# Kernel tuning notes

Measured on AMD Instinct MI355X. Metric: run time of the kernel, lower is better.

Reference implementation:

```python
import jax, jax.numpy as jnp
import numpy as np

EMO = 1024
FEAT = 1024
K = 128  # aggregation_k
H_LIST = (4, 8, 16)
D_LIST = tuple(EMO // h for h in H_LIST)  # (256, 128, 64)
D_SUM = sum(D_LIST)  # 448
H_SUM = sum(H_LIST)  # 28
N = len(H_LIST)      # 3 subspaces
TEMP = float(np.power(D_SUM, 0.5))


def _block_mask(sizes, total):
    m = np.zeros((len(sizes), total), np.float32)
    off = 0
    for i, s in enumerate(sizes):
        m[i, off:off + s] = 1.0
        off += s
    return jnp.asarray(m)

M_Q_BLK = _block_mask(D_LIST, D_SUM)  # [N, d_sum]
M_V_BLK = _block_mask(H_LIST, H_SUM)  # [N, h_sum]


def setup_inputs() -> dict:
    key = jax.random.key(0)
    ks = iter(jax.random.split(key, 32))
    nrm = lambda shape, s=1.0: jax.random.normal(next(ks), shape, jnp.float32) * s
    B, Lt, Lp, Nv = 32, 1024, 512, 256
    return {
        "emo_embedding": nrm((B, Lt, EMO)),
        "phr_feat": nrm((B, Lp, FEAT)),
        "video_feat": nrm((B, Nv, FEAT)),
        "w_v_W": nrm((FEAT, FEAT), FEAT ** -0.5), "w_v_b": nrm((FEAT,), 0.01),
        "agg_a_W": nrm((FEAT, K), FEAT ** -0.5), "agg_a_b": nrm((K,), 0.01),
        "agg_c_W": nrm((FEAT, EMO), FEAT ** -0.5), "agg_c_b": nrm((EMO,), 0.01),
        "ele_W": nrm((2 * EMO, 1), (2 * EMO) ** -0.5), "ele_b": nrm((1,), 0.01),
        "wq_W": nrm((EMO, D_SUM), EMO ** -0.5), "wq_b": nrm((D_SUM,), 0.01),
        "wk_W": nrm((EMO, D_SUM), EMO ** -0.5), "wk_b": nrm((D_SUM,), 0.01),
        "wv_W": nrm((EMO, H_SUM), EMO ** -0.5), "wv_b": nrm((H_SUM,), 0.01),
        "wr_W": nrm((EMO, N), EMO ** -0.5), "wr_b": nrm((N,), 0.01),
    }


def reference(emo_embedding, phr_feat, video_feat,
              w_v_W, w_v_b, agg_a_W, agg_a_b, agg_c_W, agg_c_b,
              ele_W, ele_b, wq_W, wq_b, wk_W, wk_b, wv_W, wv_b, wr_W, wr_b):
    B, Lt, _ = emo_embedding.shape
    Nv = video_feat.shape[1]
    Lp = phr_feat.shape[1]

    # --- feature_aggregation ---
    # AdaptiveAvgPool1d(Nv); Lp % Nv == 0 so it is an exact reshape-mean.
    phr = phr_feat.reshape(B, Nv, Lp // Nv, FEAT).mean(axis=2)
    combine = jnp.concatenate([phr @ w_v_W + w_v_b, video_feat], axis=1)   # [B, 2*Nv, FEAT]
    attn_a = jax.nn.softmax(combine @ agg_a_W + agg_a_b, axis=-1)          # [B, 2*Nv, K]
    agg_feat = jnp.einsum('bmk,bme->bke', attn_a, combine @ agg_c_W + agg_c_b)  # [B, K, EMO]

    # --- element_routing ---
    A_pool = jnp.einsum('ble,bke->blk', emo_embedding, agg_feat).mean(axis=1)   # [B, K]
    route = jnp.einsum('bk,bke->be', A_pool, agg_feat)[:, None, :]              # [B, 1, EMO]
    route = jnp.broadcast_to(route, emo_embedding.shape)
    R_e = jnp.tanh(jnp.concatenate([emo_embedding, route], axis=-1) @ ele_W + ele_b)  # [B, Lt, 1]
    route_emo = R_e * emo_embedding                                              # [B, Lt, EMO]

    # --- subspace_routing ---
    Q = route_emo @ wq_W + wq_b        # [B, Lt, d_sum]
    Kp = agg_feat @ wk_W + wk_b        # [B, K, d_sum]
    V = agg_feat @ wv_W + wv_b         # [B, K, h_sum]
    Rp = agg_feat @ wr_W + wr_b        # [B, K, N]

    # N masked copies of Q (block subspace masks); K/R are plain repeats, V is masked.
    Qm = (Q[:, None] * M_Q_BLK[None, :, None, :]).reshape(B, N * Lt, D_SUM)
    Kf = jnp.tile(Kp, (1, N, 1))                                         # [B, N*K, d_sum]
    Vf = (V[:, None] * M_V_BLK[None, :, None, :]).reshape(B, N * K, H_SUM)
    Rf = jnp.tile(Rp, (1, N, 1))                                         # [B, N*K, N]

    attn = jax.nn.softmax(jnp.einsum('bqd,bkd->bqk', Qm, Kf) / TEMP, axis=-1)  # [B, N*Lt, N*K]
    O = jnp.tanh(attn @ Vf).reshape(B, N, Lt, H_SUM)
    O_R = (attn @ Rf).reshape(B, N, Lt, N)

    # per-subspace head gating of route_emo
    T_list = []
    hoff = 0
    for i in range(N):
        hi, di = H_LIST[i], D_LIST[i]
        ori = route_emo.reshape(B, Lt, hi, di)
        Oi = O[:, i, :, hoff:hoff + hi][..., None]      # [B, Lt, hi, 1]
        T_list.append((ori * Oi).reshape(B, Lt, EMO))
        hoff += hi
    T = jnp.stack(T_list, axis=1)                        # [B, N, Lt, EMO]

    Rdiag = jnp.stack([O_R[:, j, :, j].mean(axis=-1) for j in range(N)], axis=1)  # [B, N]
    gate = jax.nn.softmax(Rdiag, axis=-1)[:, :, None, None]
    return emo_embedding + (gate * T).sum(axis=1)
```

## Files before the change

### kernel.cpp

```cpp
#include <hip/hip_runtime.h>
#include <math.h>

typedef long long i64;
typedef __attribute__((ext_vector_type(8))) short bf16x8;
typedef __attribute__((ext_vector_type(4))) float f32x4;

#define TEMP_ISQ 0.047245559f

__device__ __forceinline__ unsigned short f2b(float x) {
  union { float f; unsigned u; } a; a.f = x;
  return (unsigned short)((a.u + 0x7fffu + ((a.u >> 16) & 1u)) >> 16);
}
__device__ __forceinline__ float b2f(unsigned short b) {
  union { float f; unsigned u; } a; a.u = ((unsigned)b) << 16; return a.f;
}

template<int BIAS, int OUTM, int RS, int BZDIV>
__global__ __launch_bounds__(256)
void gemm_mfma(const unsigned short* __restrict__ Ab, i64 sA,
               const unsigned short* __restrict__ Bb, i64 sB,
               const float* __restrict__ bias,
               void* __restrict__ Ob, i64 sO,
               unsigned short* __restrict__ O2b, i64 sO2,
               int Nn, int Kd, int ldA, int ldB, int ldO,
               const float* __restrict__ rowScale, i64 sRS)
{
  __shared__ unsigned short As[8192];
  __shared__ unsigned short Bs[8192];
  const int tid = threadIdx.x;
  const int w = tid >> 6, lane = tid & 63;

  const int gx = gridDim.x, gy = gridDim.y;
  int nwg = gx * gy * gridDim.z;
  int bid = blockIdx.x + gx * (blockIdx.y + gy * blockIdx.z);
  int L = bid;
  if ((nwg & 7) == 0) L = (bid & 7) * (nwg >> 3) + (bid >> 3);
  const int bx = L % gx;
  int rem = L / gx;
  const int by = rem % gy;
  const int z  = rem / gy;

  const int m0 = by * 128, n0 = bx * 128;
  const unsigned short* A = Ab + (i64)z * sA;
  const unsigned short* B = Bb + (i64)(BZDIV == 1 ? z : z / BZDIV) * sB;
  const int wr = w >> 1, wc = w & 1;
  const int rS = tid >> 3, sS = tid & 7;
  const int cL = lane & 15, sl = lane >> 4;

  f32x4 acc[4][4];
  #pragma unroll
  for (int i = 0; i < 4; ++i)
    #pragma unroll
    for (int j = 0; j < 4; ++j) acc[i][j] = (f32x4){0.f, 0.f, 0.f, 0.f};

  for (int k0 = 0; k0 < Kd; k0 += 64) {
    #pragma unroll
    for (int q = 0; q < 4; ++q) {
      int r = rS + q * 32;
      int sg = sS ^ (r & 7);
      const unsigned short* sa = A + (i64)(m0 + r) * ldA + k0 + sg * 8;
      const unsigned short* sb = B + (i64)(n0 + r) * ldB + k0 + sg * 8;
      __builtin_amdgcn_global_load_lds(
          (__attribute__((address_space(1))) void*)sa,
          (__attribute__((address_space(3))) void*)&As[r * 64 + sS * 8], 16, 0, 0);
      __builtin_amdgcn_global_load_lds(
          (__attribute__((address_space(1))) void*)sb,
          (__attribute__((address_space(3))) void*)&Bs[r * 64 + sS * 8], 16, 0, 0);
    }
    __syncthreads();
    bf16x8 af[2][4], bfv[2][4];
    #pragma unroll
    for (int kk = 0; kk < 2; ++kk) {
      #pragma unroll
      for (int mi = 0; mi < 4; ++mi) {
        int rr = wr * 64 + mi * 16 + cL;
        int ph = (kk * 4 + sl) ^ (rr & 7);
        af[kk][mi] = *(const bf16x8*)&As[rr * 64 + ph * 8];
      }
      #pragma unroll
      for (int ni = 0; ni < 4; ++ni) {
        int rr = wc * 64 + ni * 16 + cL;
        int ph = (kk * 4 + sl) ^ (rr & 7);
        bfv[kk][ni] = *(const bf16x8*)&Bs[rr * 64 + ph * 8];
      }
    }
    #pragma unroll
    for (int kk = 0; kk < 2; ++kk)
      #pragma unroll
      for (int mi = 0; mi < 4; ++mi)
        #pragma unroll
        for (int ni = 0; ni < 4; ++ni)
          acc[mi][ni] = __builtin_amdgcn_mfma_f32_16x16x32_bf16(af[kk][mi], bfv[kk][ni], acc[mi][ni], 0, 0, 0);
    __syncthreads();
  }

  #pragma unroll
  for (int mi = 0; mi < 4; ++mi) {
    const int rowb = m0 + wr * 64 + mi * 16 + sl * 4;
    #pragma unroll
    for (int ni = 0; ni < 4; ++ni) {
      const int col = n0 + wc * 64 + ni * 16 + cL;
      if (col < Nn) {
        float bc = (BIAS == 1) ? bias[col] : 0.f;
        #pragma unroll
        for (int rg = 0; rg < 4; ++rg) {
          float v = acc[mi][ni][rg];
          if (RS) v *= rowScale[(i64)z * sRS + rowb + rg];
          v += bc;
          if (BIAS == 2) v += bias[rowb + rg];
          i64 oidx = (i64)(rowb + rg) * ldO + col;
          if (OUTM == 0)      ((float*)Ob)[(i64)z * sO + oidx] = v;
          else if (OUTM == 1) ((unsigned short*)Ob)[(i64)z * sO + oidx] = f2b(v);
          else if (OUTM == 3) ((float*)Ob)[(i64)z * sO + oidx] = tanhf(v * (1.f / 3.f));
          else {
            ((float*)Ob)[(i64)z * sO + oidx] = v;
            O2b[(i64)z * sO2 + oidx] = f2b(v);
          }
        }
      }
    }
  }
}

__global__ __launch_bounds__(256)
void emo_pass1(const float* __restrict__ emo, const float* __restrict__ eleW,
               unsigned short* __restrict__ emoB, float* __restrict__ colPart,
               float* __restrict__ dotE) {
  int b = blockIdx.y, lc = blockIdx.x;
  int t = threadIdx.x, lane = t & 63, w = t >> 6;
  float4 w4 = ((const float4*)eleW)[t];
  float4 acc = make_float4(0.f, 0.f, 0.f, 0.f);
  __shared__ float dw[64][4];
  const float4* src = (const float4*)emo + ((i64)b * 1024 + lc * 64) * 256;
  ushort4* dst = (ushort4*)emoB + ((i64)b * 1024 + lc * 64) * 256;
  for (int lr = 0; lr < 64; ++lr) {
    float4 v = src[lr * 256 + t];
    acc.x += v.x; acc.y += v.y; acc.z += v.z; acc.w += v.w;
    float d = v.x * w4.x + v.y * w4.y + v.z * w4.z + v.w * w4.w;
    #pragma unroll
    for (int o = 32; o; o >>= 1) d += __shfl_xor(d, o);
    if (!lane) dw[lr][w] = d;
    ushort4 o4; o4.x = f2b(v.x); o4.y = f2b(v.y); o4.z = f2b(v.z); o4.w = f2b(v.w);
    dst[lr * 256 + t] = o4;
  }
  __syncthreads();
  if (t < 64) dotE[(i64)b * 1024 + lc * 64 + t] = dw[t][0] + dw[t][1] + dw[t][2] + dw[t][3];
  ((float4*)colPart)[((i64)b * 16 + lc) * 256 + t] = acc;
}

__global__ void colmean2(const float* __restrict__ colPart, float* __restrict__ emomean) {
  int b = blockIdx.y, e = blockIdx.x * 256 + threadIdx.x;
  float s = 0.f;
  #pragma unroll
  for (int lc = 0; lc < 16; ++lc) s += colPart[((i64)b * 16 + lc) * 1024 + e];
  emomean[b * 1024 + e] = s * (1.f / 1024.f);
}

__global__ __launch_bounds__(256)
void transpose_w(const float* __restrict__ in, unsigned short* __restrict__ out,
                 int Kd, int N, int Npad) {
  __shared__ float T[32][33];
  int n0 = blockIdx.x * 32, k0 = blockIdx.y * 32;
  int t = threadIdx.x;
  #pragma unroll
  for (int p = 0; p < 4; ++p) {
    int idx = t + 256 * p; int kk = idx >> 5, nn = idx & 31;
    float v = 0.f;
    if (n0 + nn < N && k0 + kk < Kd) v = in[(i64)(k0 + kk) * N + (n0 + nn)];
    T[nn][kk] = v;
  }
  __syncthreads();
  #pragma unroll
  for (int p = 0; p < 4; ++p) {
    int idx = t + 256 * p; int nn = idx >> 5, kk = idx & 31;
    if (n0 + nn < Npad && k0 + kk < Kd) out[(i64)(n0 + nn) * Kd + (k0 + kk)] = f2b(T[nn][kk]);
  }
}

__global__ void kvr_bias_kernel(const float* wkb, const float* wvb, const float* wrb, float* out) {
  int t = blockIdx.x * 256 + threadIdx.x;
  if (t >= 480) return;
  out[t] = (t < 448) ? wkb[t] : (t < 476) ? wvb[t - 448] : (t < 479) ? wrb[t - 476] : 0.f;
}

__global__ void pool_phr(const float* __restrict__ phr, unsigned short* __restrict__ out) {
  i64 idx = (i64)blockIdx.x * 256 + threadIdx.x;
  if (idx >= 2097152) return;
  i64 bm = idx >> 8; int c = (int)(idx & 255);
  i64 b = bm >> 8, m = bm & 255;
  const float4* r0 = (const float4*)(phr + (b * 512 + 2 * m) * 1024) + c;
  const float4* r1 = (const float4*)(phr + (b * 512 + 2 * m + 1) * 1024) + c;
  float4 a = *r0, d = *r1;
  ushort4 o;
  o.x = f2b(0.5f * (a.x + d.x)); o.y = f2b(0.5f * (a.y + d.y));
  o.z = f2b(0.5f * (a.z + d.z)); o.w = f2b(0.5f * (a.w + d.w));
  ((ushort4*)out)[idx] = o;
}

__global__ void vconv(const float* __restrict__ video, unsigned short* __restrict__ combine) {
  i64 idx = (i64)blockIdx.x * 256 + threadIdx.x;
  if (idx >= 2097152) return;
  i64 b = idx >> 16, r = idx & 65535;
  float4 v = ((const float4*)video)[idx];
  ushort4 o;
  o.x = f2b(v.x); o.y = f2b(v.y); o.z = f2b(v.z); o.w = f2b(v.w);
  ((ushort4*)combine)[b * 131072 + 65536 + r] = o;
}

__global__ void vt_fill(const unsigned short* __restrict__ KVR, unsigned short* __restrict__ VT) {
  int b = blockIdx.y;
  int idx = blockIdx.x * 256 + threadIdx.x;
  int n = idx >> 7, k = idx & 127;
  unsigned short v = 0;
  if (n < 28) v = KVR[(i64)b * 61440 + k * 480 + 448 + n];
  VT[((i64)b * 128 + n) * 128 + k] = v;
}

__global__ void softmax_attn_a(const float* __restrict__ logits, unsigned short* __restrict__ outT) {
  int gw = (int)(((i64)blockIdx.x * blockDim.x + threadIdx.x) >> 6);
  int lane = threadIdx.x & 63;
  if (gw >= 32 * 512) return;
  int b = gw >> 9, m = gw & 511;
  const float* p = logits + (i64)gw * 128;
  float x0 = p[lane], x1 = p[lane + 64];
  float mx = fmaxf(x0, x1);
  #pragma unroll
  for (int o = 32; o; o >>= 1) mx = fmaxf(mx, __shfl_xor(mx, o));
  float e0 = expf(x0 - mx), e1 = expf(x1 - mx);
  float s = e0 + e1;
  #pragma unroll
  for (int o = 32; o; o >>= 1) s += __shfl_xor(s, o);
  float inv = 1.f / s;
  unsigned short* o0 = outT + (i64)b * 128 * 512 + m;
  o0[(i64)lane * 512] = f2b(e0 * inv);
  o0[(i64)(lane + 64) * 512] = f2b(e1 * inv);
}

__global__ void softmax_P_bf(const unsigned short* __restrict__ PL, unsigned short* __restrict__ P) {
  i64 gw = ((i64)blockIdx.x * blockDim.x + threadIdx.x) >> 6;
  int lane = threadIdx.x & 63;
  if (gw >= 98304) return;
  const unsigned short* p = PL + gw * 128;
  float x0 = b2f(p[lane]) * TEMP_ISQ, x1 = b2f(p[lane + 64]) * TEMP_ISQ;
  float mx = fmaxf(x0, x1);
  #pragma unroll
  for (int o = 32; o; o >>= 1) mx = fmaxf(mx, __shfl_xor(mx, o));
  float e0 = expf(x0 - mx), e1 = expf(x1 - mx);
  float s = e0 + e1;
  #pragma unroll
  for (int o = 32; o; o >>= 1) s += __shfl_xor(s, o);
  float inv = 1.f / s;
  P[gw * 128 + lane] = f2b(e0 * inv);
  P[gw * 128 + lane + 64] = f2b(e1 * inv);
}

__global__ void apool_kernel(const float* __restrict__ emomean, const float* __restrict__ agg,
                             float* __restrict__ Apool) {
  int gw = (int)(((i64)blockIdx.x * blockDim.x + threadIdx.x) >> 6);
  int lane = threadIdx.x & 63;
  if (gw >= 32 * 128) return;
  int b = gw >> 7, k = gw & 127;
  const float* ag = agg + ((i64)b * 128 + k) * 1024;
  const float* em = emomean + (i64)b * 1024;
  float s = 0.f;
  #pragma unroll
  for (int j = 0; j < 16; ++j) { int e = j * 64 + lane; s += em[e] * ag[e]; }
  #pragma unroll
  for (int o = 32; o; o >>= 1) s += __shfl_down(s, o);
  if (!lane) Apool[gw] = s;
}

__global__ void route1_kernel(const float* __restrict__ Apool, const float* __restrict__ agg,
                              float* __restrict__ routePart) {
  int b = blockIdx.z, kc = blockIdx.y;
  int e = blockIdx.x * 256 + threadIdx.x;
  __shared__ float Ap[32];
  if (threadIdx.x < 32) Ap[threadIdx.x] = Apool[b * 128 + kc * 32 + threadIdx.x];
  __syncthreads();
  const float* ag = agg + ((i64)b * 128 + kc * 32) * 1024 + e;
  float s = 0.f;
  #pragma unroll
  for (int k = 0; k < 32; ++k) s += Ap[k] * ag[(i64)k * 1024];
  routePart[((i64)kc * 32 + b) * 1024 + e] = s;
}
__global__ void route2_kernel(const float* __restrict__ routePart, float* __restrict__ route) {
  int b = blockIdx.y, e = blockIdx.x * 256 + threadIdx.x;
  float s = 0.f;
  #pragma unroll
  for (int kc = 0; kc < 4; ++kc) s += routePart[((i64)kc * 32 + b) * 1024 + e];
  route[b * 1024 + e] = s;
}

__global__ void rb_kernel(const float* __restrict__ route, const float* __restrict__ eleW,
                          const float* __restrict__ eleb, float* __restrict__ rb) {
  int b = blockIdx.x, t = threadIdx.x;
  float s = 0.f;
  for (int j = t; j < 1024; j += 256) s += route[b * 1024 + j] * eleW[1024 + j];
  __shared__ float red[256];
  red[t] = s; __syncthreads();
  for (int o = 128; o > 0; o >>= 1) { if (t < o) red[t] += red[t + o]; __syncthreads(); }
  if (t == 0) rb[b] = red[0] + eleb[0];
}

__global__ void re_small(const float* __restrict__ dotE, const float* __restrict__ rb,
                         float* __restrict__ Re) {
  int i = blockIdx.x * 256 + threadIdx.x;
  Re[i] = tanhf(dotE[i] + rb[i >> 10]);
}

__global__ void pmean1_kernel(const unsigned short* __restrict__ P, float* __restrict__ Ppart) {
  int bi = blockIdx.x, c = blockIdx.y, k = threadIdx.x;
  const unsigned short* p = P + ((i64)bi * 1024 + c * 128) * 128 + k;
  float s = 0.f;
  for (int l = 0; l < 128; ++l) s += b2f(p[(i64)l * 128]);
  Ppart[((i64)bi * 8 + c) * 128 + k] = s;
}
__global__ void pmean2_kernel(const float* __restrict__ Ppart, float* __restrict__ Pmean) {
  int bi = blockIdx.x, k = threadIdx.x;
  float s = 0.f;
  #pragma unroll
  for (int c = 0; c < 8; ++c) s += Ppart[((i64)bi * 8 + c) * 128 + k];
  Pmean[bi * 128 + k] = s * (1.f / 1024.f);
}

__global__ void rdiag_gate_kernel(const float* __restrict__ Pmean, const unsigned short* __restrict__ KVR,
                                  float* __restrict__ gate) {
  int b = blockIdx.x, t = threadIdx.x;
  __shared__ float red[128];
  __shared__ float rd[3];
  for (int i = 0; i < 3; ++i) {
    float v = Pmean[((i64)b * 3 + i) * 128 + t] * b2f(KVR[(i64)b * 61440 + t * 480 + 476 + i]);
    red[t] = v; __syncthreads();
    for (int o = 64; o > 0; o >>= 1) { if (t < o) red[t] += red[t + o]; __syncthreads(); }
    if (t == 0) rd[i] = red[0];
    __syncthreads();
  }
  if (t == 0) {
    float m = fmaxf(rd[0], fmaxf(rd[1], rd[2]));
    float e0 = expf(rd[0] - m), e1 = expf(rd[1] - m), e2 = expf(rd[2] - m);
    float inv = 1.f / (e0 + e1 + e2);
    gate[b * 3 + 0] = e0 * inv; gate[b * 3 + 1] = e1 * inv; gate[b * 3 + 2] = e2 * inv;
  }
}

__global__ __launch_bounds__(256)
void final_kernel(const unsigned short* __restrict__ emoB, const float* __restrict__ Re,
                  const float* __restrict__ O, const float* __restrict__ gate,
                  float* __restrict__ out) {
  i64 bl = blockIdx.x;
  int b = (int)(bl >> 10), l = (int)(bl & 1023);
  __shared__ float Gg[16];
  int t = threadIdx.x;
  if (t < 16) {
    float g0 = gate[b * 3], g1 = gate[b * 3 + 1], g2 = gate[b * 3 + 2];
    float o0 = O[((i64)(b * 3 + 0) * 1024 + l) * 28 + (t >> 2)];
    float o1 = O[((i64)(b * 3 + 1) * 1024 + l) * 28 + 4 + (t >> 1)];
    float o2 = O[((i64)(b * 3 + 2) * 1024 + l) * 28 + 12 + t];
    Gg[t] = g0 * o0 + g1 * o1 + g2 * o2;
  }
  __syncthreads();
  float re = Re[bl];
  ushort4 e4 = ((const ushort4*)(emoB + bl * 1024))[t];
  float g = 1.f + re * Gg[t >> 4];
  ((float4*)(out + bl * 1024))[t] =
      make_float4(b2f(e4.x) * g, b2f(e4.y) * g, b2f(e4.z) * g, b2f(e4.w) * g);
}

extern "C" void kernel_launch(void* const* d_in, const int* in_sizes, int n_in,
                              void* d_out, int out_size, void* d_ws, size_t ws_size,
                              hipStream_t stream) {
  const float* emo     = (const float*)d_in[0];
  const float* phr     = (const float*)d_in[1];
  const float* video   = (const float*)d_in[2];
  const float* w_v_W   = (const float*)d_in[3];
  const float* w_v_b   = (const float*)d_in[4];
  const float* agg_a_W = (const float*)d_in[5];
  const float* agg_a_b = (const float*)d_in[6];
  const float* agg_c_W = (const float*)d_in[7];
  const float* agg_c_b = (const float*)d_in[8];
  const float* ele_W   = (const float*)d_in[9];
  const float* ele_b   = (const float*)d_in[10];
  const float* wq_W    = (const float*)d_in[11];
  const float* wq_b    = (const float*)d_in[12];
  const float* wk_W    = (const float*)d_in[13];
  const float* wk_b    = (const float*)d_in[14];
  const float* wv_W    = (const float*)d_in[15];
  const float* wv_b    = (const float*)d_in[16];
  const float* wr_W    = (const float*)d_in[17];
  const float* wr_b    = (const float*)d_in[18];

  char* ws = (char*)d_ws;
  const i64 oEmoB    = 0;
  const i64 oCombine = 67108864;
  const i64 oPL      = 67108864;
  const i64 oPooled  = 100663296;
  const i64 oLogitsA = 100663296;
  const i64 oAggF    = 100663296;
  const i64 oO       = 100663296;
  const i64 oCT      = 117440512;
  const i64 oQ       = 117440512;
  const i64 oAttnAT  = 150994944;
  const i64 oAggB    = 155189248;
  const i64 oWvT     = 163577856;
  const i64 oAaT     = 165675008;
  const i64 oAcT     = 165937152;
  const i64 oWqT     = 168034304;
  const i64 oKvrT    = 169082880;
  const i64 oKVR     = 170131456;
  const i64 oVT      = 174063616;
  const i64 oKvrB    = 175112192;
  const i64 oEmomean = 175116288;
  const i64 oColPart = 175247360;
  const i64 oDotE    = 177344512;
  const i64 oApool   = 177475584;
  const i64 oRoutePt = 177491968;
  const i64 oRoute   = 178016256;
  const i64 oRb      = 178147328;
  const i64 oRe      = 178147584;
  const i64 oPpart   = 178278656;
  const i64 oPmean   = 178671872;
  const i64 oGate    = 178721024;

  unsigned short* emoB    = (unsigned short*)(ws + oEmoB);
  unsigned short* combine = (unsigned short*)(ws + oCombine);
  unsigned short* PL      = (unsigned short*)(ws + oPL);
  unsigned short* P       = PL;
  unsigned short* pooled  = (unsigned short*)(ws + oPooled);
  float*          logitsA = (float*)(ws + oLogitsA);
  float*          aggF    = (float*)(ws + oAggF);
  float*          O       = (float*)(ws + oO);
  unsigned short* CT      = (unsigned short*)(ws + oCT);
  unsigned short* Q       = (unsigned short*)(ws + oQ);
  unsigned short* attnAT  = (unsigned short*)(ws + oAttnAT);
  unsigned short* aggB    = (unsigned short*)(ws + oAggB);
  unsigned short* wvT     = (unsigned short*)(ws + oWvT);
  unsigned short* aaT     = (unsigned short*)(ws + oAaT);
  unsigned short* acT     = (unsigned short*)(ws + oAcT);
  unsigned short* wqT     = (unsigned short*)(ws + oWqT);
  unsigned short* kvrT    = (unsigned short*)(ws + oKvrT);
  unsigned short* KVR     = (unsigned short*)(ws + oKVR);
  unsigned short* VT      = (unsigned short*)(ws + oVT);
  float*          kvrB    = (float*)(ws + oKvrB);
  float*          emomean = (float*)(ws + oEmomean);
  float*          colPart = (float*)(ws + oColPart);
  float*          dotE    = (float*)(ws + oDotE);
  float*          Apool   = (float*)(ws + oApool);
  float*          routePt = (float*)(ws + oRoutePt);
  float*          route   = (float*)(ws + oRoute);
  float*          rbv     = (float*)(ws + oRb);
  float*          Re      = (float*)(ws + oRe);
  float*          Ppart   = (float*)(ws + oPpart);
  float*          Pmean   = (float*)(ws + oPmean);
  float*          gate    = (float*)(ws + oGate);

  dim3 blk(256);

  emo_pass1<<<dim3(16, 32), blk, 0, stream>>>(emo, ele_W, emoB, colPart, dotE);

  transpose_w<<<dim3(32, 32), blk, 0, stream>>>(w_v_W, wvT, 1024, 1024, 1024);
  transpose_w<<<dim3(4, 32),  blk, 0, stream>>>(agg_a_W, aaT, 1024, 128, 128);
  transpose_w<<<dim3(32, 32), blk, 0, stream>>>(agg_c_W, acT, 1024, 1024, 1024);
  transpose_w<<<dim3(16, 32), blk, 0, stream>>>(wq_W, wqT, 1024, 448, 512);
  transpose_w<<<dim3(14, 32), blk, 0, stream>>>(wk_W, kvrT, 1024, 448, 448);
  transpose_w<<<dim3(1, 32),  blk, 0, stream>>>(wv_W, kvrT + (i64)448 * 1024, 1024, 28, 28);
  transpose_w<<<dim3(2, 32),  blk, 0, stream>>>(wr_W, kvrT + (i64)476 * 1024, 1024, 3, 36);
  kvr_bias_kernel<<<2, blk, 0, stream>>>(wk_b, wv_b, wr_b, kvrB);

  pool_phr<<<8192, blk, 0, stream>>>(phr, pooled);
  vconv<<<8192, blk, 0, stream>>>(video, combine);
  gemm_mfma<1, 1, 0, 1><<<dim3(8, 2, 32), blk, 0, stream>>>(pooled, 262144, wvT, 0, w_v_b,
      (void*)combine, 524288, nullptr, 0, 1024, 1024, 1024, 1024, 1024, nullptr, 0);
  gemm_mfma<1, 0, 0, 1><<<dim3(1, 4, 32), blk, 0, stream>>>(combine, 524288, aaT, 0, agg_a_b,
      (void*)logitsA, 65536, nullptr, 0, 128, 1024, 1024, 1024, 128, nullptr, 0);
  softmax_attn_a<<<4096, blk, 0, stream>>>(logitsA, attnAT);
  gemm_mfma<2, 1, 0, 1><<<dim3(4, 8, 32), blk, 0, stream>>>(acT, 0, combine, 524288, agg_c_b,
      (void*)CT, 524288, nullptr, 0, 512, 1024, 1024, 1024, 512, nullptr, 0);
  gemm_mfma<0, 2, 0, 1><<<dim3(8, 1, 32), blk, 0, stream>>>(attnAT, 65536, CT, 524288, nullptr,
      (void*)aggF, 131072, aggB, 131072, 1024, 512, 512, 512, 1024, nullptr, 0);

  colmean2<<<dim3(4, 32), blk, 0, stream>>>(colPart, emomean);
  apool_kernel<<<1024, blk, 0, stream>>>(emomean, aggF, Apool);
  route1_kernel<<<dim3(4, 4, 32), blk, 0, stream>>>(Apool, aggF, routePt);
  route2_kernel<<<dim3(4, 32), blk, 0, stream>>>(routePt, route);
  rb_kernel<<<32, blk, 0, stream>>>(route, ele_W, ele_b, rbv);
  re_small<<<128, blk, 0, stream>>>(dotE, rbv, Re);

  gemm_mfma<1, 1, 0, 1><<<dim3(4, 1, 32), blk, 0, stream>>>(aggB, 131072, kvrT, 0, kvrB,
      (void*)KVR, 61440, nullptr, 0, 480, 1024, 1024, 1024, 480, nullptr, 0);
  vt_fill<<<dim3(64, 32), blk, 0, stream>>>(KVR, VT);
  gemm_mfma<1, 1, 1, 1><<<dim3(4, 8, 32), blk, 0, stream>>>(emoB, 1048576, wqT, 0, wq_b,
      (void*)Q, 458752, nullptr, 0, 448, 1024, 1024, 1024, 448, Re, 1024);

  const int doffs[3] = {0, 256, 384};
  const int kds[3]   = {256, 128, 64};
  for (int i = 0; i < 3; ++i) {
    gemm_mfma<0, 1, 0, 1><<<dim3(1, 8, 32), blk, 0, stream>>>(Q + doffs[i], 458752,
        KVR + doffs[i], 61440, nullptr,
        (void*)(PL + (i64)i * 131072), 393216, nullptr, 0, 128, kds[i], 448, 480, 128, nullptr, 0);
  }
  softmax_P_bf<<<24576, blk, 0, stream>>>(PL, P);
  pmean1_kernel<<<dim3(96, 8), 128, 0, stream>>>(P, Ppart);
  pmean2_kernel<<<96, 128, 0, stream>>>(Ppart, Pmean);
  gemm_mfma<0, 3, 0, 3><<<dim3(1, 8, 96), blk, 0, stream>>>(P, 131072, VT, 16384, nullptr,
      (void*)O, 28672, nullptr, 0, 28, 128, 128, 128, 28, nullptr, 0);
  rdiag_gate_kernel<<<32, 128, 0, stream>>>(Pmean, KVR, gate);
  final_kernel<<<32768, blk, 0, stream>>>(emoB, Re, O, gate, (float*)d_out);
}
```

Baseline: 472.6 us.

## Merge small kernels to cut launch count and widen emo_pass1 grid

```diff
diff --git a/kernel.cpp b/kernel.cpp
--- a/kernel.cpp
+++ b/kernel.cpp
@@ -15,7 +15,7 @@
   union { float f; unsigned u; } a; a.u = ((unsigned)b) << 16; return a.f;
 }
 
-template<int BIAS, int OUTM, int RS, int BZDIV>
+template<int BIAS, int OUTM, int RS, int BZDIV, int XMODE = 0>
 __global__ __launch_bounds__(256)
 void gemm_mfma(const unsigned short* __restrict__ Ab, i64 sA,
                const unsigned short* __restrict__ Bb, i64 sB,
@@ -23,7 +23,8 @@
                void* __restrict__ Ob, i64 sO,
                unsigned short* __restrict__ O2b, i64 sO2,
                int Nn, int Kd, int ldA, int ldB, int ldO,
-               const float* __restrict__ rowScale, i64 sRS)
+               const float* __restrict__ rowScale, i64 sRS,
+               const float* __restrict__ rsAdd)
 {
   __shared__ unsigned short As[8192];
   __shared__ unsigned short Bs[8192];
@@ -41,8 +42,20 @@
   const int z  = rem / gy;
 
   const int m0 = by * 128, n0 = bx * 128;
-  const unsigned short* A = Ab + (i64)z * sA;
-  const unsigned short* B = Bb + (i64)(BZDIV == 1 ? z : z / BZDIV) * sB;
+  const unsigned short* A;
+  const unsigned short* B;
+  int KdL = Kd;
+  if (XMODE == 1) {
+    int bb = z / 3, ii = z - bb * 3;
+    const int dof_[3] = {0, 256, 384};
+    const int kdt_[3] = {256, 128, 64};
+    A = Ab + dof_[ii] + (i64)bb * sA;
+    B = Bb + dof_[ii] + (i64)bb * sB;
+    KdL = kdt_[ii];
+  } else {
+    A = Ab + (i64)z * sA;
+    B = Bb + (i64)(BZDIV == 1 ? z : z / BZDIV) * sB;
+  }
   const int wr = w >> 1, wc = w & 1;
   const int rS = tid >> 3, sS = tid & 7;
   const int cL = lane & 15, sl = lane >> 4;
@@ -53,7 +66,7 @@
     #pragma unroll
     for (int j = 0; j < 4; ++j) acc[i][j] = (f32x4){0.f, 0.f, 0.f, 0.f};
 
-  for (int k0 = 0; k0 < Kd; k0 += 64) {
+  for (int k0 = 0; k0 < KdL; k0 += 64) {
     #pragma unroll
     for (int q = 0; q < 4; ++q) {
       int r = rS + q * 32;
@@ -105,7 +118,7 @@
         #pragma unroll
         for (int rg = 0; rg < 4; ++rg) {
           float v = acc[mi][ni][rg];
-          if (RS) v *= rowScale[(i64)z * sRS + rowb + rg];
+          if (RS) v *= tanhf(rowScale[(i64)z * sRS + rowb + rg] + rsAdd[z]);
           v += bc;
           if (BIAS == 2) v += bias[rowb + rg];
           i64 oidx = (i64)(rowb + rg) * ldO + col;
@@ -130,10 +143,11 @@
   int t = threadIdx.x, lane = t & 63, w = t >> 6;
   float4 w4 = ((const float4*)eleW)[t];
   float4 acc = make_float4(0.f, 0.f, 0.f, 0.f);
-  __shared__ float dw[64][4];
-  const float4* src = (const float4*)emo + ((i64)b * 1024 + lc * 64) * 256;
-  ushort4* dst = (ushort4*)emoB + ((i64)b * 1024 + lc * 64) * 256;
-  for (int lr = 0; lr < 64; ++lr) {
+  __shared__ float dw[16][4];
+  const float4* src = (const float4*)emo + ((i64)b * 1024 + lc * 16) * 256;
+  ushort4* dst = (ushort4*)emoB + ((i64)b * 1024 + lc * 16) * 256;
+  #pragma unroll 4
+  for (int lr = 0; lr < 16; ++lr) {
     float4 v = src[lr * 256 + t];
     acc.x += v.x; acc.y += v.y; acc.z += v.z; acc.w += v.w;
     float d = v.x * w4.x + v.y * w4.y + v.z * w4.z + v.w * w4.w;
@@ -144,36 +158,50 @@
     dst[lr * 256 + t] = o4;
   }
   __syncthreads();
-  if (t < 64) dotE[(i64)b * 1024 + lc * 64 + t] = dw[t][0] + dw[t][1] + dw[t][2] + dw[t][3];
-  ((float4*)colPart)[((i64)b * 16 + lc) * 256 + t] = acc;
+  if (t < 16) dotE[(i64)b * 1024 + lc * 16 + t] = dw[t][0] + dw[t][1] + dw[t][2] + dw[t][3];
+  ((float4*)colPart)[((i64)b * 64 + lc) * 256 + t] = acc;
 }
 
 __global__ void colmean2(const float* __restrict__ colPart, float* __restrict__ emomean) {
   int b = blockIdx.y, e = blockIdx.x * 256 + threadIdx.x;
   float s = 0.f;
-  #pragma unroll
-  for (int lc = 0; lc < 16; ++lc) s += colPart[((i64)b * 16 + lc) * 1024 + e];
+  #pragma unroll 8
+  for (int lc = 0; lc < 64; ++lc) s += colPart[((i64)b * 64 + lc) * 1024 + e];
   emomean[b * 1024 + e] = s * (1.f / 1024.f);
 }
 
 __global__ __launch_bounds__(256)
-void transpose_w(const float* __restrict__ in, unsigned short* __restrict__ out,
-                 int Kd, int N, int Npad) {
+void transpose_all(const float* __restrict__ w_v_W, const float* __restrict__ agg_a_W,
+                   const float* __restrict__ agg_c_W, const float* __restrict__ wq_W,
+                   const float* __restrict__ wk_W, const float* __restrict__ wv_W,
+                   const float* __restrict__ wr_W,
+                   unsigned short* __restrict__ wvT, unsigned short* __restrict__ aaT,
+                   unsigned short* __restrict__ acT, unsigned short* __restrict__ wqT,
+                   unsigned short* __restrict__ kvrT) {
   __shared__ float T[32][33];
-  int n0 = blockIdx.x * 32, k0 = blockIdx.y * 32;
+  int bx = blockIdx.x;
+  const float* in; unsigned short* out; int N, Npad, s0;
+  if (bx < 32)      { in = w_v_W;   out = wvT;                     N = 1024; Npad = 1024; s0 = 0; }
+  else if (bx < 36) { in = agg_a_W; out = aaT;                     N = 128;  Npad = 128;  s0 = 32; }
+  else if (bx < 68) { in = agg_c_W; out = acT;                     N = 1024; Npad = 1024; s0 = 36; }
+  else if (bx < 84) { in = wq_W;    out = wqT;                     N = 448;  Npad = 512;  s0 = 68; }
+  else if (bx < 98) { in = wk_W;    out = kvrT;                    N = 448;  Npad = 448;  s0 = 84; }
+  else if (bx < 99) { in = wv_W;    out = kvrT + (i64)448 * 1024;  N = 28;   Npad = 28;   s0 = 98; }
+  else              { in = wr_W;    out = kvrT + (i64)476 * 1024;  N = 3;    Npad = 36;   s0 = 99; }
+  int n0 = (bx - s0) * 32, k0 = blockIdx.y * 32;
   int t = threadIdx.x;
   #pragma unroll
   for (int p = 0; p < 4; ++p) {
     int idx = t + 256 * p; int kk = idx >> 5, nn = idx & 31;
     float v = 0.f;
-    if (n0 + nn < N && k0 + kk < Kd) v = in[(i64)(k0 + kk) * N + (n0 + nn)];
+    if (n0 + nn < N) v = in[(i64)(k0 + kk) * N + (n0 + nn)];
     T[nn][kk] = v;
   }
   __syncthreads();
   #pragma unroll
   for (int p = 0; p < 4; ++p) {
     int idx = t + 256 * p; int nn = idx >> 5, kk = idx & 31;
-    if (n0 + nn < Npad && k0 + kk < Kd) out[(i64)(n0 + nn) * Kd + (k0 + kk)] = f2b(T[nn][kk]);
+    if (n0 + nn < Npad) out[(i64)(n0 + nn) * 1024 + (k0 + kk)] = f2b(T[nn][kk]);
   }
 }
 
@@ -270,24 +298,17 @@
   if (!lane) Apool[gw] = s;
 }
 
-__global__ void route1_kernel(const float* __restrict__ Apool, const float* __restrict__ agg,
-                              float* __restrict__ routePart) {
-  int b = blockIdx.z, kc = blockIdx.y;
+__global__ void route_kernel(const float* __restrict__ Apool, const float* __restrict__ agg,
+                             float* __restrict__ route) {
+  int b = blockIdx.y;
   int e = blockIdx.x * 256 + threadIdx.x;
-  __shared__ float Ap[32];
-  if (threadIdx.x < 32) Ap[threadIdx.x] = Apool[b * 128 + kc * 32 + threadIdx.x];
+  __shared__ float Ap[128];
+  if (threadIdx.x < 128) Ap[threadIdx.x] = Apool[b * 128 + threadIdx.x];
   __syncthreads();
-  const float* ag = agg + ((i64)b * 128 + kc * 32) * 1024 + e;
+  const float* ag = agg + (i64)b * 128 * 1024 + e;
   float s = 0.f;
-  #pragma unroll
-  for (int k = 0; k < 32; ++k) s += Ap[k] * ag[(i64)k * 1024];
-  routePart[((i64)kc * 32 + b) * 1024 + e] = s;
-}
-__global__ void route2_kernel(const float* __restrict__ routePart, float* __restrict__ route) {
-  int b = blockIdx.y, e = blockIdx.x * 256 + threadIdx.x;
-  float s = 0.f;
-  #pragma unroll
-  for (int kc = 0; kc < 4; ++kc) s += routePart[((i64)kc * 32 + b) * 1024 + e];
+  #pragma unroll 8
+  for (int k = 0; k < 128; ++k) s += Ap[k] * ag[(i64)k * 1024];
   route[b * 1024 + e] = s;
 }
 
@@ -302,12 +323,6 @@
   if (t == 0) rb[b] = red[0] + eleb[0];
 }
 
-__global__ void re_small(const float* __restrict__ dotE, const float* __restrict__ rb,
-                         float* __restrict__ Re) {
-  int i = blockIdx.x * 256 + threadIdx.x;
-  Re[i] = tanhf(dotE[i] + rb[i >> 10]);
-}
-
 __global__ void pmean1_kernel(const unsigned short* __restrict__ P, float* __restrict__ Ppart) {
   int bi = blockIdx.x, c = blockIdx.y, k = threadIdx.x;
   const unsigned short* p = P + ((i64)bi * 1024 + c * 128) * 128 + k;
@@ -315,21 +330,17 @@
   for (int l = 0; l < 128; ++l) s += b2f(p[(i64)l * 128]);
   Ppart[((i64)bi * 8 + c) * 128 + k] = s;
 }
-__global__ void pmean2_kernel(const float* __restrict__ Ppart, float* __restrict__ Pmean) {
-  int bi = blockIdx.x, k = threadIdx.x;
-  float s = 0.f;
-  #pragma unroll
-  for (int c = 0; c < 8; ++c) s += Ppart[((i64)bi * 8 + c) * 128 + k];
-  Pmean[bi * 128 + k] = s * (1.f / 1024.f);
-}
-
-__global__ void rdiag_gate_kernel(const float* __restrict__ Pmean, const unsigned short* __restrict__ KVR,
-                                  float* __restrict__ gate) {
+
+__global__ void pmean2_rdiag(const float* __restrict__ Ppart, const unsigned short* __restrict__ KVR,
+                             float* __restrict__ gate) {
   int b = blockIdx.x, t = threadIdx.x;
   __shared__ float red[128];
   __shared__ float rd[3];
   for (int i = 0; i < 3; ++i) {
-    float v = Pmean[((i64)b * 3 + i) * 128 + t] * b2f(KVR[(i64)b * 61440 + t * 480 + 476 + i]);
+    float s = 0.f;
+    #pragma unroll
+    for (int c = 0; c < 8; ++c) s += Ppart[((i64)(b * 3 + i) * 8 + c) * 128 + t];
+    float v = s * (1.f / 1024.f) * b2f(KVR[(i64)b * 61440 + t * 480 + 476 + i]);
     red[t] = v; __syncthreads();
     for (int o = 64; o > 0; o >>= 1) { if (t < o) red[t] += red[t + o]; __syncthreads(); }
     if (t == 0) rd[i] = red[0];
@@ -344,9 +355,9 @@
 }
 
 __global__ __launch_bounds__(256)
-void final_kernel(const unsigned short* __restrict__ emoB, const float* __restrict__ Re,
-                  const float* __restrict__ O, const float* __restrict__ gate,
-                  float* __restrict__ out) {
+void final_kernel(const unsigned short* __restrict__ emoB, const float* __restrict__ dotE,
+                  const float* __restrict__ rbv, const float* __restrict__ O,
+                  const float* __restrict__ gate, float* __restrict__ out) {
   i64 bl = blockIdx.x;
   int b = (int)(bl >> 10), l = (int)(bl & 1023);
   __shared__ float Gg[16];
@@ -359,7 +370,7 @@
     Gg[t] = g0 * o0 + g1 * o1 + g2 * o2;
   }
   __syncthreads();
-  float re = Re[bl];
+  float re = tanhf(dotE[bl] + rbv[b]);
   ushort4 e4 = ((const ushort4*)(emoB + bl * 1024))[t];
   float g = 1.f + re * Gg[t >> 4];
   ((float4*)(out + bl * 1024))[t] =
@@ -411,15 +422,12 @@
   const i64 oKvrB    = 175112192;
   const i64 oEmomean = 175116288;
   const i64 oColPart = 175247360;
-  const i64 oDotE    = 177344512;
-  const i64 oApool   = 177475584;
-  const i64 oRoutePt = 177491968;
-  const i64 oRoute   = 178016256;
-  const i64 oRb      = 178147328;
-  const i64 oRe      = 178147584;
-  const i64 oPpart   = 178278656;
-  const i64 oPmean   = 178671872;
-  const i64 oGate    = 178721024;
+  const i64 oDotE    = 183635968;
+  const i64 oApool   = 183767040;
+  const i64 oRoute   = 183783424;
+  const i64 oRb      = 183914496;
+  const i64 oPpart   = 183914752;
+  const i64 oGate    = 184307968;
 
   unsigned short* emoB    = (unsigned short*)(ws + oEmoB);
   unsigned short* combine = (unsigned short*)(ws + oCombine);
@@ -445,64 +453,49 @@
   float*          colPart = (float*)(ws + oColPart);
   float*          dotE    = (float*)(ws + oDotE);
   float*          Apool   = (float*)(ws + oApool);
-  float*          routePt = (float*)(ws + oRoutePt);
   float*          route   = (float*)(ws + oRoute);
   float*          rbv     = (float*)(ws + oRb);
-  float*          Re      = (float*)(ws + oRe);
   float*          Ppart   = (float*)(ws + oPpart);
-  float*          Pmean   = (float*)(ws + oPmean);
   float*          gate    = (float*)(ws + oGate);
 
   dim3 blk(256);
 
-  emo_pass1<<<dim3(16, 32), blk, 0, stream>>>(emo, ele_W, emoB, colPart, dotE);
-
-  transpose_w<<<dim3(32, 32), blk, 0, stream>>>(w_v_W, wvT, 1024, 1024, 1024);
-  transpose_w<<<dim3(4, 32),  blk, 0, stream>>>(agg_a_W, aaT, 1024, 128, 128);
-  transpose_w<<<dim3(32, 32), blk, 0, stream>>>(agg_c_W, acT, 1024, 1024, 1024);
-  transpose_w<<<dim3(16, 32), blk, 0, stream>>>(wq_W, wqT, 1024, 448, 512);
-  transpose_w<<<dim3(14, 32), blk, 0, stream>>>(wk_W, kvrT, 1024, 448, 448);
-  transpose_w<<<dim3(1, 32),  blk, 0, stream>>>(wv_W, kvrT + (i64)448 * 1024, 1024, 28, 28);
-  transpose_w<<<dim3(2, 32),  blk, 0, stream>>>(wr_W, kvrT + (i64)476 * 1024, 1024, 3, 36);
+  emo_pass1<<<dim3(64, 32), blk, 0, stream>>>(emo, ele_W, emoB, colPart, dotE);
+
+  transpose_all<<<dim3(101, 32), blk, 0, stream>>>(w_v_W, agg_a_W, agg_c_W, wq_W, wk_W, wv_W, wr_W,
+                                                   wvT, aaT, acT, wqT, kvrT);
   kvr_bias_kernel<<<2, blk, 0, stream>>>(wk_b, wv_b, wr_b, kvrB);
 
   pool_phr<<<8192, blk, 0, stream>>>(phr, pooled);
   vconv<<<8192, blk, 0, stream>>>(video, combine);
   gemm_mfma<1, 1, 0, 1><<<dim3(8, 2, 32), blk, 0, stream>>>(pooled, 262144, wvT, 0, w_v_b,
-      (void*)combine, 524288, nullptr, 0, 1024, 1024, 1024, 1024, 1024, nullptr, 0);
+      (void*)combine, 524288, nullptr, 0, 1024, 1024, 1024, 1024, 1024, nullptr, 0, nullptr);
   gemm_mfma<1, 0, 0, 1><<<dim3(1, 4, 32), blk, 0, stream>>>(combine, 524288, aaT, 0, agg_a_b,
-      (void*)logitsA, 65536, nullptr, 0, 128, 1024, 1024, 1024, 128, nullptr, 0);
+      (void*)logitsA, 65536, nullptr, 0, 128, 1024, 1024, 1024, 128, nullptr, 0, nullptr);
   softmax_attn_a<<<4096, blk, 0, stream>>>(logitsA, attnAT);
   gemm_mfma<2, 1, 0, 1><<<dim3(4, 8, 32), blk, 0, stream>>>(acT, 0, combine, 524288, agg_c_b,
-      (void*)CT, 524288, nullptr, 0, 512, 1024, 1024, 1024, 512, nullptr, 0);
+      (void*)CT, 524288, nullptr, 0, 512, 1024, 1024, 1024, 512, nullptr, 0, nullptr);
   gemm_mfma<0, 2, 0, 1><<<dim3(8, 1, 32), blk, 0, stream>>>(attnAT, 65536, CT, 524288, nullptr,
-      (void*)aggF, 131072, aggB, 131072, 1024, 512, 512, 512, 1024, nullptr, 0);
+      (void*)aggF, 131072, aggB, 131072, 1024, 512, 512, 512, 1024, nullptr, 0, nullptr);
 
   colmean2<<<dim3(4, 32), blk, 0, stream>>>(colPart, emomean);
   apool_kernel<<<1024, blk, 0, stream>>>(emomean, aggF, Apool);
-  route1_kernel<<<dim3(4, 4, 32), blk, 0, stream>>>(Apool, aggF, routePt);
-  route2_kernel<<<dim3(4, 32), blk, 0, stream>>>(routePt, route);
+  route_kernel<<<dim3(4, 32), blk, 0, stream>>>(Apool, aggF, route);
   rb_kernel<<<32, blk, 0, stream>>>(route, ele_W, ele_b, rbv);
-  re_small<<<128, blk, 0, stream>>>(dotE, rbv, Re);
 
   gemm_mfma<1, 1, 0, 1><<<dim3(4, 1, 32), blk, 0, stream>>>(aggB, 131072, kvrT, 0, kvrB,
-      (void*)KVR, 61440, nullptr, 0, 480, 1024, 1024, 1024, 480, nullptr, 0);
+      (void*)KVR, 61440, nullptr, 0, 480, 1024, 1024, 1024, 480, nullptr, 0, nullptr);
   vt_fill<<<dim3(64, 32), blk, 0, stream>>>(KVR, VT);
   gemm_mfma<1, 1, 1, 1><<<dim3(4, 8, 32), blk, 0, stream>>>(emoB, 1048576, wqT, 0, wq_b,
-      (void*)Q, 458752, nullptr, 0, 448, 1024, 1024, 1024, 448, Re, 1024);
-
-  const int doffs[3] = {0, 256, 384};
-  const int kds[3]   = {256, 128, 64};
-  for (int i = 0; i < 3; ++i) {
-    gemm_mfma<0, 1, 0, 1><<<dim3(1, 8, 32), blk, 0, stream>>>(Q + doffs[i], 458752,
-        KVR + doffs[i], 61440, nullptr,
-        (void*)(PL + (i64)i * 131072), 393216, nullptr, 0, 128, kds[i], 448, 480, 128, nullptr, 0);
-  }
+      (void*)Q, 458752, nullptr, 0, 448, 1024, 1024, 1024, 448, dotE, 1024, rbv);
+
+  gemm_mfma<0, 1, 0, 1, 1><<<dim3(1, 8, 96), blk, 0, stream>>>(Q, 458752, KVR, 61440, nullptr,
+      (void*)PL, 131072, nullptr, 0, 128, 0, 448, 480, 128, nullptr, 0, nullptr);
+
   softmax_P_bf<<<24576, blk, 0, stream>>>(PL, P);
   pmean1_kernel<<<dim3(96, 8), 128, 0, stream>>>(P, Ppart);
-  pmean2_kernel<<<96, 128, 0, stream>>>(Ppart, Pmean);
   gemm_mfma<0, 3, 0, 3><<<dim3(1, 8, 96), blk, 0, stream>>>(P, 131072, VT, 16384, nullptr,
-      (void*)O, 28672, nullptr, 0, 28, 128, 128, 128, 28, nullptr, 0);
-  rdiag_gate_kernel<<<32, 128, 0, stream>>>(Pmean, KVR, gate);
-  final_kernel<<<32768, blk, 0, stream>>>(emoB, Re, O, gate, (float*)d_out);
-}
+      (void*)O, 28672, nullptr, 0, 28, 128, 128, 128, 28, nullptr, 0, nullptr);
+  pmean2_rdiag<<<32, 128, 0, stream>>>(Ppart, KVR, gate);
+  final_kernel<<<32768, blk, 0, stream>>>(emoB, dotE, rbv, O, gate, (float*)d_out);
+}
```

Result: faster. 453.0 us (-4.1%).
